# Kernel tuning notes

Hardware: AMD Instinct MI355X
Metric: run time of the kernel (lower is better)

Reference implementation:

```python
import jax, jax.numpy as jnp
import numpy as np

MARGIN = 1.0
N, D, P = 4096, 768, 100

def setup_inputs() -> dict:
    key = jax.random.key(0)
    k1, k2, k3 = jax.random.split(key, 3)
    inputs = jax.random.normal(k1, (N, D), dtype=jnp.float32)
    targets = jax.random.randint(k2, (N,), 0, P)
    center = jax.random.normal(k3, (P, D), dtype=jnp.float32)
    return {"inputs": inputs, "targets": targets, "center": center}

def reference(inputs, targets, center):
    n = inputs.shape[0]
    # pairwise euclidean distances: ||xi||^2 + ||xj||^2 - 2 xi.xj
    sq = jnp.sum(inputs * inputs, axis=1)                      # [n]
    dist = sq[:, None] + sq[None, :] - 2.0 * (inputs @ inputs.T)
    dist = jnp.sqrt(jnp.clip(dist, 1e-12))                     # [n, n]
    mask = targets[:, None] == targets[None, :]                # same-class mask
    inf = jnp.asarray(jnp.inf, dist.dtype)
    # hardest positive: max over same-class (diagonal always True -> finite)
    dist_ap = jnp.max(jnp.where(mask, dist, -inf), axis=1)     # [n]
    # hardest negative: min over different-class, fallback ap+margin if none
    dist_an = jnp.min(jnp.where(mask, inf, dist), axis=1)      # [n]
    has_neg = jnp.any(~mask, axis=1)
    dist_an = jnp.where(has_neg, dist_an, dist_ap + MARGIN)
    # prototype augmentation: row-normalized centers, min distance to any center
    cn = center / jnp.linalg.norm(center, axis=1, keepdims=True)
    csq = jnp.sum(cn * cn, axis=1)                             # [P]
    d2c = sq[:, None] + csq[None, :] - 2.0 * (inputs @ cn.T)   # [n, P]
    d2c = jnp.clip(jnp.sqrt(jnp.clip(d2c, 0.0)), 1e-12)
    dist_an = jnp.minimum(dist_an, jnp.min(d2c, axis=1))
    # MarginRankingLoss(dist_an, dist_ap, y=1) = mean(relu(margin - (an - ap)))
    return jnp.mean(jax.nn.relu(MARGIN + dist_ap - dist_an))
```

## Files before the change

### kernel.cpp

```cpp
#include <hip/hip_runtime.h>
#include <math.h>

#define N_ 4096
#define D_ 768
#define P_ 100
#define PPAD 128
#define NT 24
#define NTRI 528
#define NBLK 560

typedef __attribute__((ext_vector_type(8))) short short8;
typedef __attribute__((ext_vector_type(4))) float f32x4;

typedef const __attribute__((address_space(1))) void* gld_src_t;
typedef __attribute__((address_space(3))) void* gld_dst_t;
#define GLOAD16(g, d) __builtin_amdgcn_global_load_lds((gld_src_t)(g), (gld_dst_t)(d), 16, 0, 0)

#define WAITVM4() asm volatile("s_waitcnt vmcnt(4)" ::: "memory")
#define WAITVM0() asm volatile("s_waitcnt vmcnt(0)" ::: "memory")
static __device__ __forceinline__ void barrier_fenced() {
    asm volatile("" ::: "memory");
    __builtin_amdgcn_s_barrier();
    asm volatile("" ::: "memory");
}

__device__ inline unsigned short f2bf(float f) {
    union { float f; unsigned int u; } v; v.f = f;
    unsigned int u = v.u + 0x7fffu + ((v.u >> 16) & 1u);
    return (unsigned short)(u >> 16);
}

__global__ __launch_bounds__(256) void pre_kernel(
    const float* __restrict__ X, const float* __restrict__ C,
    float* __restrict__ sq, unsigned short* __restrict__ Xbf,
    unsigned short* __restrict__ cnbf, float* __restrict__ csq) {
    const int gw = blockIdx.x * 4 + (threadIdx.x >> 6);
    const int l = threadIdx.x & 63;
    if (gw < N_) {
        const float4* x4 = (const float4*)(X + (size_t)gw * D_);
        short4* ob = (short4*)(Xbf + (size_t)gw * D_);
        float s = 0.f;
#pragma unroll
        for (int c = 0; c < 3; ++c) {
            float4 v = x4[c * 64 + l];
            s = fmaf(v.x, v.x, fmaf(v.y, v.y, fmaf(v.z, v.z, fmaf(v.w, v.w, s))));
            short4 o;
            o.x = (short)f2bf(v.x); o.y = (short)f2bf(v.y);
            o.z = (short)f2bf(v.z); o.w = (short)f2bf(v.w);
            ob[c * 64 + l] = o;
        }
#pragma unroll
        for (int m = 1; m < 64; m <<= 1) s += __shfl_xor(s, m);
        if (l == 0) sq[gw] = s;
    } else {
        const int p = gw - N_;
        if (p >= PPAD) return;
        short4* ob = (short4*)(cnbf + (size_t)p * D_);
        if (p < P_) {
            const float4* c4 = (const float4*)(C + (size_t)p * D_);
            float4 v[3];
            float s = 0.f;
#pragma unroll
            for (int c = 0; c < 3; ++c) {
                v[c] = c4[c * 64 + l];
                s = fmaf(v[c].x, v[c].x, fmaf(v[c].y, v[c].y,
                    fmaf(v[c].z, v[c].z, fmaf(v[c].w, v[c].w, s))));
            }
#pragma unroll
            for (int m = 1; m < 64; m <<= 1) s += __shfl_xor(s, m);
            float rn = 1.0f / sqrtf(s);
#pragma unroll
            for (int c = 0; c < 3; ++c) {
                short4 o;
                o.x = (short)f2bf(v[c].x * rn); o.y = (short)f2bf(v[c].y * rn);
                o.z = (short)f2bf(v[c].z * rn); o.w = (short)f2bf(v[c].w * rn);
                ob[c * 64 + l] = o;
            }
            if (l == 0) csq[p] = s * rn * rn;
        } else {
            short4 z; z.x = z.y = z.z = z.w = 0;
#pragma unroll
            for (int c = 0; c < 3; ++c) ob[c * 64 + l] = z;
            if (l == 0) csq[p] = 1e30f;
        }
    }
}

__global__ __launch_bounds__(256, 3) void mfma_kernel(
    const unsigned short* __restrict__ Xbf, const unsigned short* __restrict__ cnbf,
    const int* __restrict__ T, const float* __restrict__ sq,
    const float* __restrict__ csq,
    float* __restrict__ ap_part, float* __restrict__ an_part,
    float* __restrict__ minc) {
    __shared__ __align__(16) unsigned short lds[3 * 8192];

    const int tid = threadIdx.x;
    const int l = tid & 63;
    const int w = tid >> 6;
    const int wr = w >> 1;
    const int wc = w & 1;

    const int orig = blockIdx.x;
    const int bid = (orig & 7) * 70 + (orig >> 3);
    int it, jt;
    if (bid < NTRI) {
        int t = (int)((sqrtf(8.0f * bid + 1.0f) - 1.0f) * 0.5f);
        t += ((t + 1) * (t + 2) / 2 <= bid);
        t -= (t * (t + 1) / 2 > bid);
        it = t; jt = bid - t * (t + 1) / 2;
    } else { it = bid - NTRI; jt = 32; }
    const bool is_center = (jt == 32);
    const bool is_diag = (it == jt);
    const int i0 = it * 128;
    const int j0 = is_center ? 0 : jt * 128;
    const unsigned short* __restrict__ Bmat = is_center ? cnbf : Xbf;

    const int srow = tid >> 2;
    const int scol = ((tid & 3) * 8) ^ (((srow & 6) >> 1) << 3);
    const unsigned short* gA0 = Xbf + (size_t)(i0 + srow) * D_ + scol;
    const unsigned short* gA1 = gA0 + (size_t)64 * D_;
    const unsigned short* gB0 = Bmat + (size_t)(j0 + srow) * D_ + scol;
    const unsigned short* gB1 = gB0 + (size_t)64 * D_;
    const int dA0 = w * 512, dA1 = 2048 + w * 512;
    const int dB0 = 4096 + w * 512, dB1 = 6144 + w * 512;

    const int col = l & 15;
    const int hi = l >> 4;
    const int rko = (hi * 8) ^ ((l & 6) << 2);
    const int aro = (wr * 64 + col) * 32 + rko;
    const int bro = 4096 + (wc * 64 + col) * 32 + rko;

    f32x4 acc[4][4];
#pragma unroll
    for (int m = 0; m < 4; ++m)
#pragma unroll
        for (int n = 0; n < 4; ++n) acc[m][n] = (f32x4){0.f, 0.f, 0.f, 0.f};

#define STAGE(t)                                                     \
    do {                                                             \
        const int bo_ = ((t) % 3) * 8192;                            \
        const int ke_ = (t) * 32;                                    \
        GLOAD16(gA0 + ke_, &lds[bo_ + dA0]);                         \
        GLOAD16(gA1 + ke_, &lds[bo_ + dA1]);                         \
        GLOAD16(gB0 + ke_, &lds[bo_ + dB0]);                         \
        GLOAD16(gB1 + ke_, &lds[bo_ + dB1]);                         \
    } while (0)

    STAGE(0);
    STAGE(1);
    WAITVM4();
    barrier_fenced();

    int bo = 0;
    for (int t = 0; t < NT; ++t) {
        if (t + 2 < NT) STAGE(t + 2);
        const unsigned short* Lb = &lds[bo * 8192];
        short8 a[4], b[4];
#pragma unroll
        for (int m = 0; m < 4; ++m)
            a[m] = *reinterpret_cast<const short8*>(Lb + aro + m * 512);
#pragma unroll
        for (int n = 0; n < 4; ++n)
            b[n] = *reinterpret_cast<const short8*>(Lb + bro + n * 512);
        __builtin_amdgcn_s_setprio(1);
#pragma unroll
        for (int m = 0; m < 4; ++m)
#pragma unroll
            for (int n = 0; n < 4; ++n)
                acc[m][n] = __builtin_amdgcn_mfma_f32_16x16x32_bf16(a[m], b[n], acc[m][n], 0, 0, 0);
        __builtin_amdgcn_s_setprio(0);
        if (t < NT - 1) {
            if (t + 2 < NT) WAITVM4();
            else WAITVM0();
            barrier_fenced();
        }
        bo = (bo == 2) ? 0 : bo + 1;
    }
#undef STAGE

    float* lf = (float*)lds;
    __syncthreads();

    if (!is_center) {
        float sqj[4]; int tj[4];
#pragma unroll
        for (int n = 0; n < 4; ++n) {
            int j = j0 + wc * 64 + n * 16 + col;
            sqj[n] = sq[j];
            tj[n] = T[j];
        }
        float apC[4], anC[4];
#pragma unroll
        for (int n = 0; n < 4; ++n) { apC[n] = -1e30f; anC[n] = 1e30f; }

#pragma unroll
        for (int m = 0; m < 4; ++m) {
#pragma unroll
            for (int r = 0; r < 4; ++r) {
                const int lrow = wr * 64 + m * 16 + hi * 4 + r;
                const int i = i0 + lrow;
                float sqi = sq[i];
                int ti = T[i];
                float apR = -1e30f, anR = 1e30f;
#pragma unroll
                for (int n = 0; n < 4; ++n) {
                    float d2 = sqi + sqj[n] - 2.0f * acc[m][n][r];
                    float d = sqrtf(fmaxf(d2, 1e-12f));
                    bool same = (tj[n] == ti);
                    apR = same ? fmaxf(apR, d) : apR;
                    anR = same ? anR : fminf(anR, d);
                    apC[n] = same ? fmaxf(apC[n], d) : apC[n];
                    anC[n] = same ? anC[n] : fminf(anC[n], d);
                }
#pragma unroll
                for (int msk = 1; msk < 16; msk <<= 1) {
                    apR = fmaxf(apR, __shfl_xor(apR, msk));
                    anR = fminf(anR, __shfl_xor(anR, msk));
                }
                if (col == 0) {
                    lf[wc * 128 + lrow] = apR;
                    lf[256 + wc * 128 + lrow] = anR;
                }
            }
        }
        __syncthreads();
        if (tid < 128) {
            float a = fmaxf(lf[tid], lf[128 + tid]);
            float b = fminf(lf[256 + tid], lf[384 + tid]);
            ap_part[(size_t)jt * N_ + i0 + tid] = a;
            an_part[(size_t)jt * N_ + i0 + tid] = b;
        }

        if (!is_diag) {
            __syncthreads();
#pragma unroll
            for (int n = 0; n < 4; ++n) {
                apC[n] = fmaxf(apC[n], __shfl_xor(apC[n], 16));
                apC[n] = fmaxf(apC[n], __shfl_xor(apC[n], 32));
                anC[n] = fminf(anC[n], __shfl_xor(anC[n], 16));
                anC[n] = fminf(anC[n], __shfl_xor(anC[n], 32));
                if (hi == 0) {
                    int jl = wc * 64 + n * 16 + col;
                    lf[wr * 128 + jl] = apC[n];
                    lf[256 + wr * 128 + jl] = anC[n];
                }
            }
            __syncthreads();
            if (tid < 128) {
                float a = fmaxf(lf[tid], lf[128 + tid]);
                float b = fminf(lf[256 + tid], lf[384 + tid]);
                ap_part[(size_t)(32 + it) * N_ + j0 + tid] = a;
                an_part[(size_t)(32 + it) * N_ + j0 + tid] = b;
            }
        }
    } else {
        float sqj[4];
#pragma unroll
        for (int n = 0; n < 4; ++n) sqj[n] = csq[wc * 64 + n * 16 + col];
#pragma unroll
        for (int m = 0; m < 4; ++m) {
#pragma unroll
            for (int r = 0; r < 4; ++r) {
                const int lrow = wr * 64 + m * 16 + hi * 4 + r;
                const int i = i0 + lrow;
                float sqi = sq[i];
                float mc = 1e30f;
#pragma unroll
                for (int n = 0; n < 4; ++n) {
                    float d2 = sqi + sqj[n] - 2.0f * acc[m][n][r];
                    float d = fmaxf(sqrtf(fmaxf(d2, 0.0f)), 1e-12f);
                    mc = fminf(mc, d);
                }
#pragma unroll
                for (int msk = 1; msk < 16; msk <<= 1)
                    mc = fminf(mc, __shfl_xor(mc, msk));
                if (col == 0) lf[wc * 128 + lrow] = mc;
            }
        }
        __syncthreads();
        if (tid < 128) minc[i0 + tid] = fminf(lf[tid], lf[128 + tid]);
    }
}

__global__ __launch_bounds__(256) void combine1(
    const float* __restrict__ ap_part, const float* __restrict__ an_part,
    const float* __restrict__ minc, float* __restrict__ bsum) {
    __shared__ float sred[4];
    const int i = blockIdx.x * 256 + threadIdx.x;
    const int r = i >> 7;
    float ap = -1e30f, an = 1e30f;
    for (int jt = 0; jt <= r; ++jt) {
        ap = fmaxf(ap, ap_part[(size_t)jt * N_ + i]);
        an = fminf(an, an_part[(size_t)jt * N_ + i]);
    }
    for (int it2 = r + 1; it2 < 32; ++it2) {
        ap = fmaxf(ap, ap_part[(size_t)(32 + it2) * N_ + i]);
        an = fminf(an, an_part[(size_t)(32 + it2) * N_ + i]);
    }
    float dan = (an < 1e29f) ? an : (ap + 1.0f);
    dan = fminf(dan, minc[i]);
    float term = fmaxf(0.0f, 1.0f + ap - dan);
#pragma unroll
    for (int m = 32; m > 0; m >>= 1) term += __shfl_xor(term, m);
    if ((threadIdx.x & 63) == 0) sred[threadIdx.x >> 6] = term;
    __syncthreads();
    if (threadIdx.x == 0)
        bsum[blockIdx.x] = sred[0] + sred[1] + sred[2] + sred[3];
}

__global__ void finalize(const float* __restrict__ bsum, float* __restrict__ out) {
    if (threadIdx.x == 0) {
        float s = 0.f;
        for (int b = 0; b < N_ / 256; ++b) s += bsum[b];
        out[0] = s / (float)N_;
    }
}

extern "C" void kernel_launch(void* const* d_in, const int* in_sizes, int n_in,
                              void* d_out, int out_size, void* d_ws, size_t ws_size,
                              hipStream_t stream) {
    const float* X = (const float*)d_in[0];
    const int* T = (const int*)d_in[1];
    const float* C = (const float*)d_in[2];
    float* out = (float*)d_out;

    float* ws = (float*)d_ws;
    float* sq = ws;
    float* csq = ws + 4096;
    float* minc = ws + 4224;
    float* bsum = ws + 8320;
    unsigned short* Xbf = (unsigned short*)(ws + 8336);
    unsigned short* cnbf = (unsigned short*)(ws + 1581200);
    float* ap_part = ws + 1630352;
    float* an_part = ws + 1892496;

    pre_kernel<<<(N_ + PPAD) / 4, 256, 0, stream>>>(X, C, sq, Xbf, cnbf, csq);
    mfma_kernel<<<NBLK, 256, 0, stream>>>(Xbf, cnbf, T, sq, csq, ap_part, an_part, minc);
    combine1<<<N_ / 256, 256, 0, stream>>>(ap_part, an_part, minc, bsum);
    finalize<<<1, 64, 0, stream>>>(bsum, out);
}
```

Measured before the change: 61.68 us.

## Reorder GEMM main loop, group tiles per XCD, widen combine reduction

The main loop now issues LDS reads, then the next global-to-LDS stage, waits on LDS and the barrier, and only then runs the MFMAs. It also drops setprio and unrolls the loop by 3. Tile decoding now groups blocks into 8x8 super-tile regions per XCD slot, aiming for better L2 reuse of the A and B rows. The combine step gives each row of partials to a wavefront (lanes read the ap/an partials in parallel and shuffle-reduce) and uses 256 blocks instead of 16. A 256-thread finalize replaces the serial one, and the bsum workspace grows, shifting the later buffer offsets.

```diff
diff --git a/kernel.cpp b/kernel.cpp
--- a/kernel.cpp
+++ b/kernel.cpp
@@ -18,16 +18,35 @@
 
 #define WAITVM4() asm volatile("s_waitcnt vmcnt(4)" ::: "memory")
 #define WAITVM0() asm volatile("s_waitcnt vmcnt(0)" ::: "memory")
-static __device__ __forceinline__ void barrier_fenced() {
-    asm volatile("" ::: "memory");
-    __builtin_amdgcn_s_barrier();
-    asm volatile("" ::: "memory");
-}
+#define WAITLGKM0() asm volatile("s_waitcnt lgkmcnt(0)" ::: "memory")
 
 __device__ inline unsigned short f2bf(float f) {
     union { float f; unsigned int u; } v; v.f = f;
     unsigned int u = v.u + 0x7fffu + ((v.u >> 16) & 1u);
     return (unsigned short)(u >> 16);
+}
+
+static __device__ __forceinline__ void decode_tile(int orig, int* pit, int* pjt) {
+    const int x = orig & 7;
+    const int k = orig >> 3;
+    if (k >= 66) { *pit = x * 4 + (k - 66); *pjt = 32; return; }
+    const int g = x * 66 + k;
+    const int cumR[11] = {0, 36, 100, 136, 200, 264, 300, 364, 428, 492, 528};
+    const int GIr[10] = {0, 1, 1, 2, 2, 2, 3, 3, 3, 3};
+    const int GJr[10] = {0, 0, 1, 0, 1, 2, 0, 1, 2, 3};
+    int r = 0;
+    while (cumR[r + 1] <= g) ++r;
+    const int u = g - cumR[r];
+    int di, dj;
+    if (GIr[r] == GJr[r]) {
+        di = 0;
+        while ((di + 1) * (di + 2) / 2 <= u) ++di;
+        dj = u - di * (di + 1) / 2;
+    } else {
+        di = u >> 3; dj = u & 7;
+    }
+    *pit = GIr[r] * 8 + di;
+    *pjt = GJr[r] * 8 + dj;
 }
 
 __global__ __launch_bounds__(256) void pre_kernel(
@@ -100,17 +119,9 @@
     const int wr = w >> 1;
     const int wc = w & 1;
 
-    const int orig = blockIdx.x;
-    const int bid = (orig & 7) * 70 + (orig >> 3);
     int it, jt;
-    if (bid < NTRI) {
-        int t = (int)((sqrtf(8.0f * bid + 1.0f) - 1.0f) * 0.5f);
-        t += ((t + 1) * (t + 2) / 2 <= bid);
-        t -= (t * (t + 1) / 2 > bid);
-        it = t; jt = bid - t * (t + 1) / 2;
-    } else { it = bid - NTRI; jt = 32; }
+    decode_tile(blockIdx.x, &it, &jt);
     const bool is_center = (jt == 32);
-    const bool is_diag = (it == jt);
     const int i0 = it * 128;
     const int j0 = is_center ? 0 : jt * 128;
     const unsigned short* __restrict__ Bmat = is_center ? cnbf : Xbf;
@@ -149,11 +160,12 @@
     STAGE(0);
     STAGE(1);
     WAITVM4();
-    barrier_fenced();
+    __builtin_amdgcn_s_barrier();
+    __builtin_amdgcn_sched_barrier(0);
 
     int bo = 0;
+#pragma unroll 3
     for (int t = 0; t < NT; ++t) {
-        if (t + 2 < NT) STAGE(t + 2);
         const unsigned short* Lb = &lds[bo * 8192];
         short8 a[4], b[4];
 #pragma unroll
@@ -162,18 +174,20 @@
 #pragma unroll
         for (int n = 0; n < 4; ++n)
             b[n] = *reinterpret_cast<const short8*>(Lb + bro + n * 512);
-        __builtin_amdgcn_s_setprio(1);
-#pragma unroll
-        for (int m = 0; m < 4; ++m)
-#pragma unroll
-            for (int n = 0; n < 4; ++n)
-                acc[m][n] = __builtin_amdgcn_mfma_f32_16x16x32_bf16(a[m], b[n], acc[m][n], 0, 0, 0);
-        __builtin_amdgcn_s_setprio(0);
+        if (t + 2 < NT) STAGE(t + 2);
+        WAITLGKM0();
         if (t < NT - 1) {
             if (t + 2 < NT) WAITVM4();
             else WAITVM0();
-            barrier_fenced();
-        }
+            __builtin_amdgcn_s_barrier();
+            __builtin_amdgcn_sched_barrier(0);
+        }
+#pragma unroll
+        for (int m = 0; m < 4; ++m)
+#pragma unroll
+            for (int n = 0; n < 4; ++n)
+                acc[m][n] = __builtin_amdgcn_mfma_f32_16x16x32_bf16(
+                    a[m], b[n], acc[m][n], 0, 0, 0);
         bo = (bo == 2) ? 0 : bo + 1;
     }
 #undef STAGE
@@ -231,7 +245,7 @@
             an_part[(size_t)jt * N_ + i0 + tid] = b;
         }
 
-        if (!is_diag) {
+        if (it != jt) {
             __syncthreads();
 #pragma unroll
             for (int n = 0; n < 4; ++n) {
@@ -282,38 +296,45 @@
     }
 }
 
-__global__ __launch_bounds__(256) void combine1(
+__global__ __launch_bounds__(256) void combine2(
     const float* __restrict__ ap_part, const float* __restrict__ an_part,
     const float* __restrict__ minc, float* __restrict__ bsum) {
+    const int w = threadIdx.x >> 6;
+    const int l = threadIdx.x & 63;
+    const int l2 = l & 31;
+    float wsum = 0.f;
+#pragma unroll
+    for (int q = 0; q < 4; ++q) {
+        const int i = blockIdx.x * 16 + w * 4 + q;
+        const int r = i >> 7;
+        const int s = (l2 <= r) ? l2 : 32 + l2;
+        float v = (l < 32) ? ap_part[(size_t)s * N_ + i]
+                           : an_part[(size_t)s * N_ + i];
+#pragma unroll
+        for (int m = 1; m < 32; m <<= 1) {
+            float o = __shfl_xor(v, m);
+            v = (l < 32) ? fmaxf(v, o) : fminf(v, o);
+        }
+        float ap = __shfl(v, 0);
+        float an = __shfl(v, 32);
+        float dan = (an < 1e29f) ? an : (ap + 1.0f);
+        dan = fminf(dan, minc[i]);
+        wsum += fmaxf(0.0f, 1.0f + ap - dan);
+    }
+    if (l == 0) bsum[blockIdx.x * 4 + w] = wsum;
+}
+
+__global__ __launch_bounds__(256) void finalize(
+    const float* __restrict__ bsum, float* __restrict__ out) {
     __shared__ float sred[4];
-    const int i = blockIdx.x * 256 + threadIdx.x;
-    const int r = i >> 7;
-    float ap = -1e30f, an = 1e30f;
-    for (int jt = 0; jt <= r; ++jt) {
-        ap = fmaxf(ap, ap_part[(size_t)jt * N_ + i]);
-        an = fminf(an, an_part[(size_t)jt * N_ + i]);
-    }
-    for (int it2 = r + 1; it2 < 32; ++it2) {
-        ap = fmaxf(ap, ap_part[(size_t)(32 + it2) * N_ + i]);
-        an = fminf(an, an_part[(size_t)(32 + it2) * N_ + i]);
-    }
-    float dan = (an < 1e29f) ? an : (ap + 1.0f);
-    dan = fminf(dan, minc[i]);
-    float term = fmaxf(0.0f, 1.0f + ap - dan);
-#pragma unroll
-    for (int m = 32; m > 0; m >>= 1) term += __shfl_xor(term, m);
-    if ((threadIdx.x & 63) == 0) sred[threadIdx.x >> 6] = term;
+    const int tid = threadIdx.x;
+    float s = bsum[tid] + bsum[tid + 256] + bsum[tid + 512] + bsum[tid + 768];
+#pragma unroll
+    for (int m = 32; m > 0; m >>= 1) s += __shfl_xor(s, m);
+    if ((tid & 63) == 0) sred[tid >> 6] = s;
     __syncthreads();
-    if (threadIdx.x == 0)
-        bsum[blockIdx.x] = sred[0] + sred[1] + sred[2] + sred[3];
-}
-
-__global__ void finalize(const float* __restrict__ bsum, float* __restrict__ out) {
-    if (threadIdx.x == 0) {
-        float s = 0.f;
-        for (int b = 0; b < N_ / 256; ++b) s += bsum[b];
-        out[0] = s / (float)N_;
-    }
+    if (tid == 0)
+        out[0] = (sred[0] + sred[1] + sred[2] + sred[3]) / (float)N_;
 }
 
 extern "C" void kernel_launch(void* const* d_in, const int* in_sizes, int n_in,
@@ -329,13 +350,13 @@
     float* csq = ws + 4096;
     float* minc = ws + 4224;
     float* bsum = ws + 8320;
-    unsigned short* Xbf = (unsigned short*)(ws + 8336);
-    unsigned short* cnbf = (unsigned short*)(ws + 1581200);
-    float* ap_part = ws + 1630352;
-    float* an_part = ws + 1892496;
+    unsigned short* Xbf = (unsigned short*)(ws + 9344);
+    unsigned short* cnbf = (unsigned short*)(ws + 1582208);
+    float* ap_part = ws + 1631360;
+    float* an_part = ws + 1893504;
 
     pre_kernel<<<(N_ + PPAD) / 4, 256, 0, stream>>>(X, C, sq, Xbf, cnbf, csq);
     mfma_kernel<<<NBLK, 256, 0, stream>>>(Xbf, cnbf, T, sq, csq, ap_part, an_part, minc);
-    combine1<<<N_ / 256, 256, 0, stream>>>(ap_part, an_part, minc, bsum);
-    finalize<<<1, 64, 0, stream>>>(bsum, out);
-}
+    combine2<<<N_ / 16, 256, 0, stream>>>(ap_part, an_part, minc, bsum);
+    finalize<<<1, 256, 0, stream>>>(bsum, out);
+}
```

Result: faster. 50.79 us, median of 3 (-17.7%).
